# Kernel tuning notes

Measured on AMD Instinct MI355X. Metric: run time of the kernel, lower is better.

## Reference

```python
import jax, jax.numpy as jnp
import numpy as np

H = 16  # num_heads

def setup_inputs() -> dict:
    key = jax.random.key(0)
    k1, k2, k3 = jax.random.split(key, 3)
    D = 1024
    x = jax.random.normal(k1, (4, 2048, D), dtype=jnp.float32)
    W_qkv = jax.random.normal(k2, (D, 3 * D), dtype=jnp.float32) * (1.0 / np.sqrt(D))
    b_qkv = jnp.zeros((3 * D,), dtype=jnp.float32)
    W_out = jax.random.normal(k3, (D, D), dtype=jnp.float32) * (1.0 / np.sqrt(D))
    b_out = jnp.zeros((D,), dtype=jnp.float32)
    return {"x": x, "W_qkv": W_qkv, "b_qkv": b_qkv, "W_out": W_out, "b_out": b_out}

def reference(x, W_qkv, b_qkv, W_out, b_out):
    B, S, D = x.shape
    hd = D // H  # head_dim
    qkv = x @ W_qkv + b_qkv  # [B,S,3D]
    q, k, v = jnp.split(qkv, 3, axis=-1)
    # [B,S,D] -> [B,H,S,hd]
    q = q.reshape(B, S, H, hd).transpose(0, 2, 1, 3)
    k = k.reshape(B, S, H, hd).transpose(0, 2, 1, 3)
    v = v.reshape(B, S, H, hd).transpose(0, 2, 1, 3)
    scores = jnp.einsum('bhqd,bhkd->bhqk', q, k) / jnp.sqrt(jnp.float32(hd))
    weights = jax.nn.softmax(scores, axis=-1)  # dropout p=0.0 (eval)
    out = jnp.einsum('bhqk,bhkd->bhqd', weights, v)
    out = out.transpose(0, 2, 1, 3).reshape(B, S, D)
    return out @ W_out + b_out
```

## Files before the change

### kernel.cpp

```cpp
#include <hip/hip_runtime.h>

typedef __bf16 bf16;
typedef __bf16 bf16x8 __attribute__((ext_vector_type(8)));
typedef __bf16 bf16x4 __attribute__((ext_vector_type(4)));
typedef float f32x4 __attribute__((ext_vector_type(4)));

static constexpr int NB = 4;
static constexpr int NS = 2048;
static constexpr int ND = 1024;
static constexpr int NH = 16;
static constexpr int HD = 64;
static constexpr float QSCALE = 0.18033688011112042f;

#define GL16(g, l)                                                             \
    __builtin_amdgcn_global_load_lds(                                          \
        (const __attribute__((address_space(1))) void*)(g),                    \
        (__attribute__((address_space(3))) void*)(l), 16, 0, 0)

__global__ void k_conv(const float* __restrict__ in, bf16* __restrict__ out, int n) {
    int i = (blockIdx.x * blockDim.x + threadIdx.x) * 4;
    if (i < n) {
        float4 v = *reinterpret_cast<const float4*>(in + i);
        bf16* o = out + i;
        o[0] = (bf16)v.x; o[1] = (bf16)v.y; o[2] = (bf16)v.z; o[3] = (bf16)v.w;
    }
}

__global__ void k_transconv(const float* __restrict__ in, bf16* __restrict__ out,
                            int K, int N) {
    __shared__ float tile[32][33];
    int k0 = blockIdx.y * 32, n0 = blockIdx.x * 32;
    int tx = threadIdx.x, ty = threadIdx.y;
    for (int j = 0; j < 32; j += 8)
        tile[ty + j][tx] = in[(long)(k0 + ty + j) * N + n0 + tx];
    __syncthreads();
    for (int j = 0; j < 32; j += 8)
        out[(long)(n0 + ty + j) * K + k0 + tx] = (bf16)tile[tx][ty + j];
}

template <int EPI>
__global__ __launch_bounds__(256, 2) void k_gemm(
    const bf16* __restrict__ A, const bf16* __restrict__ Bt,
    const float* __restrict__ bias,
    void* __restrict__ out0, void* __restrict__ out1, void* __restrict__ out2,
    int M, int N, int Kd)
{
    constexpr int BM = 128, BN = 128, BK = 64;
    __shared__ __align__(16) bf16 As[2][BM * BK];
    __shared__ __align__(16) bf16 Bs[2][BN * BK];

    const int t = threadIdx.x;
    const int wid = t >> 6, lane = t & 63;
    const int wm = wid >> 1, wn = wid & 1;
    const int m0 = blockIdx.y * BM, n0 = blockIdx.x * BN;
    const int lrow = lane & 15, lhi = lane >> 4;

    const int srow0 = wid * 32 + (lane >> 3);
    const int scol = ((lane & 7) ^ (lane >> 3)) * 8;
    const bf16* ag = A + (long)(m0 + srow0) * Kd + scol;
    const bf16* bg = Bt + (long)(n0 + srow0) * Kd + scol;

    auto STAGE = [&](int buf_, int k0_) {
#pragma unroll
        for (int c = 0; c < 4; ++c) {
            GL16(ag + (long)(c * 8) * Kd + k0_, &As[buf_][(wid * 32 + c * 8) * BK]);
            GL16(bg + (long)(c * 8) * Kd + k0_, &Bs[buf_][(wid * 32 + c * 8) * BK]);
        }
    };

    f32x4 acc[4][4] = {};
    const int nt = Kd >> 6;
    const int swzr = (lrow & 7) << 4;
    int co[2];
#pragma unroll
    for (int kk = 0; kk < 2; ++kk)
        co[kk] = ((kk * 64 + lhi * 16) ^ swzr) >> 1;

    STAGE(0, 0);
    __syncthreads();
    int cur = 0;
    for (int tix = 0; tix < nt; ++tix) {
        if (tix + 1 < nt) STAGE(cur ^ 1, (tix + 1) * BK);

        bf16x8 af[2][4], bfr[2][4];
#pragma unroll
        for (int kk = 0; kk < 2; ++kk)
#pragma unroll
            for (int i = 0; i < 4; ++i) {
                af[kk][i]  = *reinterpret_cast<const bf16x8*>(
                    &As[cur][(wm * 64 + i * 16 + lrow) * BK + co[kk]]);
                bfr[kk][i] = *reinterpret_cast<const bf16x8*>(
                    &Bs[cur][(wn * 64 + i * 16 + lrow) * BK + co[kk]]);
            }
        __builtin_amdgcn_s_setprio(1);
#pragma unroll
        for (int kk = 0; kk < 2; ++kk)
#pragma unroll
            for (int i = 0; i < 4; ++i)
#pragma unroll
                for (int j = 0; j < 4; ++j)
                    acc[i][j] = __builtin_amdgcn_mfma_f32_16x16x32_bf16(
                        af[kk][i], bfr[kk][j], acc[i][j], 0, 0, 0);
        __builtin_amdgcn_s_setprio(0);
        __syncthreads();
        cur ^= 1;
    }

    if (EPI == 0) {
        bf16* Qb = (bf16*)out0; bf16* Kb = (bf16*)out1; bf16* Vt = (bf16*)out2;
#pragma unroll
        for (int j = 0; j < 4; ++j) {
            int col = n0 + wn * 64 + j * 16 + lrow;
            float bv = bias[col];
            int which = col >> 10;
            int rem = col & 1023;
            int h = rem >> 6, d = rem & 63;
#pragma unroll
            for (int i = 0; i < 4; ++i) {
                int mbase = m0 + wm * 64 + i * 16 + lhi * 4;
#pragma unroll
                for (int r = 0; r < 4; ++r) {
                    int row = mbase + r;
                    int bb = row >> 11, s = row & 2047;
                    long bh = bb * NH + h;
                    float v = acc[i][j][r] + bv;
                    if (which == 0)      Qb[(bh * NS + s) * HD + d] = (bf16)(v * QSCALE);
                    else if (which == 1) Kb[(bh * NS + s) * HD + d] = (bf16)v;
                    else                 Vt[(bh * HD + d) * NS + s] = (bf16)v;
                }
            }
        }
    } else {
        float* O = (float*)out0;
#pragma unroll
        for (int j = 0; j < 4; ++j) {
            int col = n0 + wn * 64 + j * 16 + lrow;
            float bv = bias[col];
#pragma unroll
            for (int i = 0; i < 4; ++i) {
                int mbase = m0 + wm * 64 + i * 16 + lhi * 4;
#pragma unroll
                for (int r = 0; r < 4; ++r)
                    O[(long)(mbase + r) * N + col] = acc[i][j][r] + bv;
            }
        }
    }
}

__global__ __launch_bounds__(256, 2) void k_attn(
    const bf16* __restrict__ Qb, const bf16* __restrict__ Kb,
    const bf16* __restrict__ Vt, bf16* __restrict__ Ao)
{
    constexpr int KB = 64;
    constexpr int NT = NS / KB;
    __shared__ bf16 Ks[2][KB * HD];
    __shared__ bf16 Vs[2][HD * KB];
    __shared__ bf16 Ps[4][16][72];

    const int t = threadIdx.x;
    const int wid = t >> 6, lane = t & 63;
    const int lrow = lane & 15, lhi = lane >> 4;

    const int flat = blockIdx.y * gridDim.x + blockIdx.x;
    const int n = (flat & 7) * 256 + (flat >> 3);
    const int bh = n >> 5;
    const int q0 = (n & 31) * 64 + wid * 16;

    const bf16* Qg = Qb + ((long)bh * NS + q0) * HD;
    const bf16* Kg = Kb + (long)bh * NS * HD;
    const bf16* Vg = Vt + (long)bh * HD * NS;

    bf16x8 qf[2];
#pragma unroll
    for (int c = 0; c < 2; ++c)
        qf[c] = *reinterpret_cast<const bf16x8*>(Qg + (long)lrow * HD + c * 32 + lhi * 8);

    f32x4 of[4] = {};
    float lsum = 0.f;

    const int sr  = t >> 2;
    const int scb = (t & 3) << 5;
    const int swz = (sr & 7) << 4;
    const int se0 = sr * 64 + ((scb ^ swz) >> 1);
    const int se1 = sr * 64 + (((scb + 16) ^ swz) >> 1);

    bf16x8 k0, k1, v0, v1;
#define LOADREGS(kb_)                                                          \
    {                                                                          \
        const bf16* kp = Kg + (long)((kb_) + sr) * HD + (scb >> 1);            \
        k0 = *reinterpret_cast<const bf16x8*>(kp);                             \
        k1 = *reinterpret_cast<const bf16x8*>(kp + 8);                         \
        const bf16* vp = Vg + (long)sr * NS + (kb_) + (scb >> 1);              \
        v0 = *reinterpret_cast<const bf16x8*>(vp);                             \
        v1 = *reinterpret_cast<const bf16x8*>(vp + 8);                         \
    }
#define WRITEBUF(b_)                                                           \
    {                                                                          \
        *reinterpret_cast<bf16x8*>(&Ks[b_][se0]) = k0;                         \
        *reinterpret_cast<bf16x8*>(&Ks[b_][se1]) = k1;                         \
        *reinterpret_cast<bf16x8*>(&Vs[b_][se0]) = v0;                         \
        *reinterpret_cast<bf16x8*>(&Vs[b_][se1]) = v1;                         \
    }

    LOADREGS(0);
    __syncthreads();
    WRITEBUF(0);
    LOADREGS(KB);

    for (int i = 0; i < NT; ++i) {
        __syncthreads();
        if (i + 1 < NT) WRITEBUF((i + 1) & 1);
        if (i + 2 < NT) LOADREGS((i + 2) * KB);
        const int b = i & 1;

        f32x4 st[4] = {};
        __builtin_amdgcn_s_setprio(1);
#pragma unroll
        for (int j = 0; j < 4; ++j) {
            const int row = j * 16 + lrow;
            const int rb = row * 64, rs = (row & 7) << 4;
#pragma unroll
            for (int c = 0; c < 2; ++c) {
                const int colb = c * 64 + lhi * 16;
                bf16x8 kf = *reinterpret_cast<const bf16x8*>(&Ks[b][rb + ((colb ^ rs) >> 1)]);
                st[j] = __builtin_amdgcn_mfma_f32_16x16x32_bf16(kf, qf[c], st[j], 0, 0, 0);
            }
        }
        __builtin_amdgcn_s_setprio(0);

#pragma unroll
        for (int j = 0; j < 4; ++j) {
            bf16x4 pk;
#pragma unroll
            for (int r = 0; r < 4; ++r) {
                float p = __builtin_amdgcn_exp2f(st[j][r]);
                lsum += p;
                pk[r] = (bf16)p;
            }
            *reinterpret_cast<bf16x4*>(&Ps[wid][lrow][j * 16 + 4 * lhi]) = pk;
        }

        __builtin_amdgcn_s_setprio(1);
#pragma unroll
        for (int chunk = 0; chunk < 2; ++chunk) {
            bf16x8 pf = *reinterpret_cast<const bf16x8*>(&Ps[wid][lrow][chunk * 32 + lhi * 8]);
#pragma unroll
            for (int f = 0; f < 4; ++f) {
                const int row = f * 16 + lrow;
                const int rb = row * 64, rs = (row & 7) << 4;
                const int colb = chunk * 64 + lhi * 16;
                bf16x8 vf = *reinterpret_cast<const bf16x8*>(&Vs[b][rb + ((colb ^ rs) >> 1)]);
                of[f] = __builtin_amdgcn_mfma_f32_16x16x32_bf16(pf, vf, of[f], 0, 0, 0);
            }
        }
        __builtin_amdgcn_s_setprio(0);
    }
#undef LOADREGS
#undef WRITEBUF

    lsum += __shfl_xor(lsum, 16);
    lsum += __shfl_xor(lsum, 32);
    float inv[4];
#pragma unroll
    for (int r = 0; r < 4; ++r)
        inv[r] = 1.0f / __shfl(lsum, 4 * lhi + r);

    const int bb = bh >> 4, h = bh & 15;
#pragma unroll
    for (int f = 0; f < 4; ++f) {
        int d = f * 16 + lrow;
#pragma unroll
        for (int r = 0; r < 4; ++r) {
            int s = q0 + 4 * lhi + r;
            Ao[((long)bb * NS + s) * ND + h * HD + d] = (bf16)(of[f][r] * inv[r]);
        }
    }
}

extern "C" void kernel_launch(void* const* d_in, const int* in_sizes, int n_in,
                              void* d_out, int out_size, void* d_ws, size_t ws_size,
                              hipStream_t stream) {
    const float* x    = (const float*)d_in[0];
    const float* Wqkv = (const float*)d_in[1];
    const float* bqkv = (const float*)d_in[2];
    const float* Wout = (const float*)d_in[3];
    const float* bout = (const float*)d_in[4];
    float* out = (float*)d_out;

    char* ws = (char*)d_ws;
    bf16* Xb  = (bf16*)(ws);
    bf16* Wqt = (bf16*)(ws + 16777216);
    bf16* Wot = (bf16*)(ws + 23068672);
    bf16* Qb  = (bf16*)(ws + 25165824);
    bf16* Kb  = (bf16*)(ws + 41943040);
    bf16* Vt  = (bf16*)(ws + 58720256);
    bf16* Ab  = (bf16*)(ws + 75497472);

    k_conv<<<dim3(8192), dim3(256), 0, stream>>>(x, Xb, NB * NS * ND);
    k_transconv<<<dim3(96, 32), dim3(32, 8), 0, stream>>>(Wqkv, Wqt, ND, 3 * ND);
    k_transconv<<<dim3(32, 32), dim3(32, 8), 0, stream>>>(Wout, Wot, ND, ND);

    k_gemm<0><<<dim3(24, 64), dim3(256), 0, stream>>>(
        Xb, Wqt, bqkv, Qb, Kb, Vt, NB * NS, 3 * ND, ND);

    k_attn<<<dim3(NS / 64, NB * NH), dim3(256), 0, stream>>>(Qb, Kb, Vt, Ab);

    k_gemm<1><<<dim3(8, 64), dim3(256), 0, stream>>>(
        Ab, Wot, bout, out, nullptr, nullptr, NB * NS, ND, ND);
}
```

Before: 224.3 us.

## Reshape P fragment in registers via permlane swaps instead of LDS round-trip

The attention kernel no longer writes exp'd scores to a shared-memory P buffer and reads them back as MFMA A-operand fragments. It packs pairs into bf16x2 words and rearranges them across lanes with permlane32_swap and xor-16 shuffles. This removes the per-tile LDS store/load and shared footprint, and launch bounds are raised to 4 blocks per SM to take advantage of the lower LDS use. In exchange it adds cross-lane shuffle instructions and tighter register limits, which could cause spills.

```diff
diff --git a/kernel.cpp b/kernel.cpp
--- a/kernel.cpp
+++ b/kernel.cpp
@@ -4,6 +4,7 @@
 typedef __bf16 bf16x8 __attribute__((ext_vector_type(8)));
 typedef __bf16 bf16x4 __attribute__((ext_vector_type(4)));
 typedef float f32x4 __attribute__((ext_vector_type(4)));
+typedef unsigned u32x2 __attribute__((ext_vector_type(2)));
 
 static constexpr int NB = 4;
 static constexpr int NS = 2048;
@@ -16,6 +17,12 @@
     __builtin_amdgcn_global_load_lds(                                          \
         (const __attribute__((address_space(1))) void*)(g),                    \
         (__attribute__((address_space(3))) void*)(l), 16, 0, 0)
+
+static __device__ __forceinline__ unsigned pk2(float a, float b) {
+    union { __bf16 h[2]; unsigned u; } t;
+    t.h[0] = (__bf16)a; t.h[1] = (__bf16)b;
+    return t.u;
+}
 
 __global__ void k_conv(const float* __restrict__ in, bf16* __restrict__ out, int n) {
     int i = (blockIdx.x * blockDim.x + threadIdx.x) * 4;
@@ -147,7 +154,7 @@
     }
 }
 
-__global__ __launch_bounds__(256, 2) void k_attn(
+__global__ __launch_bounds__(256, 4) void k_attn(
     const bf16* __restrict__ Qb, const bf16* __restrict__ Kb,
     const bf16* __restrict__ Vt, bf16* __restrict__ Ao)
 {
@@ -155,7 +162,6 @@
     constexpr int NT = NS / KB;
     __shared__ bf16 Ks[2][KB * HD];
     __shared__ bf16 Vs[2][HD * KB];
-    __shared__ bf16 Ps[4][16][72];
 
     const int t = threadIdx.x;
     const int wid = t >> 6, lane = t & 63;
@@ -228,32 +234,43 @@
         }
         __builtin_amdgcn_s_setprio(0);
 
+        unsigned pa[4], pb[4];
 #pragma unroll
         for (int j = 0; j < 4; ++j) {
-            bf16x4 pk;
-#pragma unroll
-            for (int r = 0; r < 4; ++r) {
-                float p = __builtin_amdgcn_exp2f(st[j][r]);
-                lsum += p;
-                pk[r] = (bf16)p;
-            }
-            *reinterpret_cast<bf16x4*>(&Ps[wid][lrow][j * 16 + 4 * lhi]) = pk;
-        }
-
-        __builtin_amdgcn_s_setprio(1);
-#pragma unroll
-        for (int chunk = 0; chunk < 2; ++chunk) {
-            bf16x8 pf = *reinterpret_cast<const bf16x8*>(&Ps[wid][lrow][chunk * 32 + lhi * 8]);
+            float e0 = __builtin_amdgcn_exp2f(st[j][0]);
+            float e1 = __builtin_amdgcn_exp2f(st[j][1]);
+            float e2 = __builtin_amdgcn_exp2f(st[j][2]);
+            float e3 = __builtin_amdgcn_exp2f(st[j][3]);
+            lsum += (e0 + e1) + (e2 + e3);
+            pa[j] = pk2(e0, e1);
+            pb[j] = pk2(e2, e3);
+        }
+
+        const bool sel = (lhi & 1) != 0;
+#pragma unroll
+        for (int c = 0; c < 2; ++c) {
+            u32x2 sa = __builtin_amdgcn_permlane32_swap(pa[2 * c], pa[2 * c + 1], false, false);
+            u32x2 sb = __builtin_amdgcn_permlane32_swap(pb[2 * c], pb[2 * c + 1], false, false);
+            unsigned Za = sa[0], Wa = sa[1], Zb = sb[0], Wb = sb[1];
+            unsigned Zas = __shfl_xor((int)Za, 16), Was = __shfl_xor((int)Wa, 16);
+            unsigned Zbs = __shfl_xor((int)Zb, 16), Wbs = __shfl_xor((int)Wb, 16);
+            union { unsigned u[4]; bf16x8 v; } frag;
+            frag.u[0] = sel ? Was : Za;
+            frag.u[1] = sel ? Wbs : Zb;
+            frag.u[2] = sel ? Wa : Zas;
+            frag.u[3] = sel ? Wb : Zbs;
+
+            __builtin_amdgcn_s_setprio(1);
 #pragma unroll
             for (int f = 0; f < 4; ++f) {
                 const int row = f * 16 + lrow;
                 const int rb = row * 64, rs = (row & 7) << 4;
-                const int colb = chunk * 64 + lhi * 16;
+                const int colb = c * 64 + lhi * 16;
                 bf16x8 vf = *reinterpret_cast<const bf16x8*>(&Vs[b][rb + ((colb ^ rs) >> 1)]);
-                of[f] = __builtin_amdgcn_mfma_f32_16x16x32_bf16(pf, vf, of[f], 0, 0, 0);
-            }
-        }
-        __builtin_amdgcn_s_setprio(0);
+                of[f] = __builtin_amdgcn_mfma_f32_16x16x32_bf16(frag.v, vf, of[f], 0, 0, 0);
+            }
+            __builtin_amdgcn_s_setprio(0);
+        }
     }
 #undef LOADREGS
 #undef WRITEBUF
```

New measurement: 232.5 us. 3.6% more time.

## Restructure attention: 32 queries per wave, async LDS staging, register-resident P

Applied to the files above, without the earlier changes.

The attention kernel now gives each wave 32 query rows instead of 16, so every K/V fragment read from LDS feeds two MFMAs. K/V tiles are staged straight into LDS with global_load_lds rather than through registers. P stays in registers and feeds 16x16x16 MFMAs, which removes the per-wave LDS round trip for P. Output stores are vectorised and launch bounds are raised to 4 blocks per CU. The cost is higher register pressure from doubled accumulators under the tighter occupancy bound, and a grid remap that halves the block count.

```diff
diff --git a/kernel.cpp b/kernel.cpp
--- a/kernel.cpp
+++ b/kernel.cpp
@@ -3,6 +3,7 @@
 typedef __bf16 bf16;
 typedef __bf16 bf16x8 __attribute__((ext_vector_type(8)));
 typedef __bf16 bf16x4 __attribute__((ext_vector_type(4)));
+typedef short s16x4 __attribute__((ext_vector_type(4)));
 typedef float f32x4 __attribute__((ext_vector_type(4)));
 
 static constexpr int NB = 4;
@@ -16,6 +17,12 @@
     __builtin_amdgcn_global_load_lds(                                          \
         (const __attribute__((address_space(1))) void*)(g),                    \
         (__attribute__((address_space(3))) void*)(l), 16, 0, 0)
+
+static __device__ __forceinline__ unsigned pk2(float a, float b) {
+    union { __bf16 h[2]; unsigned u; } t;
+    t.h[0] = (__bf16)a; t.h[1] = (__bf16)b;
+    return t.u;
+}
 
 __global__ void k_conv(const float* __restrict__ in, bf16* __restrict__ out, int n) {
     int i = (blockIdx.x * blockDim.x + threadIdx.x) * 4;
@@ -147,132 +154,130 @@
     }
 }
 
-__global__ __launch_bounds__(256, 2) void k_attn(
+__global__ __launch_bounds__(256, 4) void k_attn(
     const bf16* __restrict__ Qb, const bf16* __restrict__ Kb,
     const bf16* __restrict__ Vt, bf16* __restrict__ Ao)
 {
     constexpr int KB = 64;
     constexpr int NT = NS / KB;
-    __shared__ bf16 Ks[2][KB * HD];
-    __shared__ bf16 Vs[2][HD * KB];
-    __shared__ bf16 Ps[4][16][72];
+    __shared__ __align__(16) bf16 Ks[2][KB * HD];
+    __shared__ __align__(16) bf16 Vs[2][HD * KB];
 
     const int t = threadIdx.x;
     const int wid = t >> 6, lane = t & 63;
     const int lrow = lane & 15, lhi = lane >> 4;
 
     const int flat = blockIdx.y * gridDim.x + blockIdx.x;
-    const int n = (flat & 7) * 256 + (flat >> 3);
-    const int bh = n >> 5;
-    const int q0 = (n & 31) * 64 + wid * 16;
-
-    const bf16* Qg = Qb + ((long)bh * NS + q0) * HD;
+    const int n = (flat & 7) * 128 + (flat >> 3);
+    const int bh = n >> 4;
+    const int qblk = (n & 15) * 128;
+    const int qw = qblk + wid * 32;
+
+    const bf16* Qg = Qb + ((long)bh * NS + qw) * HD;
     const bf16* Kg = Kb + (long)bh * NS * HD;
     const bf16* Vg = Vt + (long)bh * HD * NS;
 
-    bf16x8 qf[2];
-#pragma unroll
-    for (int c = 0; c < 2; ++c)
-        qf[c] = *reinterpret_cast<const bf16x8*>(Qg + (long)lrow * HD + c * 32 + lhi * 8);
-
-    f32x4 of[4] = {};
-    float lsum = 0.f;
-
-    const int sr  = t >> 2;
-    const int scb = (t & 3) << 5;
-    const int swz = (sr & 7) << 4;
-    const int se0 = sr * 64 + ((scb ^ swz) >> 1);
-    const int se1 = sr * 64 + (((scb + 16) ^ swz) >> 1);
-
-    bf16x8 k0, k1, v0, v1;
-#define LOADREGS(kb_)                                                          \
+    bf16x8 qf[2][2];
+#pragma unroll
+    for (int qfr = 0; qfr < 2; ++qfr)
+#pragma unroll
+        for (int c = 0; c < 2; ++c)
+            qf[qfr][c] = *reinterpret_cast<const bf16x8*>(
+                Qg + (long)(qfr * 16 + lrow) * HD + c * 32 + lhi * 8);
+
+    f32x4 of[2][4] = {};
+    float lsum[2] = {0.f, 0.f};
+
+    const int gsr = lane >> 3;
+    const int gsc = ((lane & 7) ^ gsr) * 8;
+    auto STAGE = [&](int buf, int kb) {
+#pragma unroll
+        for (int c = 0; c < 2; ++c) {
+            const int rb = wid * 16 + c * 8;
+            GL16(Kg + (long)(kb + rb + gsr) * HD + gsc, &Ks[buf][rb * 64]);
+            GL16(Vg + (long)(rb + gsr) * NS + kb + gsc, &Vs[buf][rb * 64]);
+        }
+    };
+
+    const int rsw = (lrow & 7) << 4;
+
+#define COMPUTE(b_, i_)                                                        \
     {                                                                          \
-        const bf16* kp = Kg + (long)((kb_) + sr) * HD + (scb >> 1);            \
-        k0 = *reinterpret_cast<const bf16x8*>(kp);                             \
-        k1 = *reinterpret_cast<const bf16x8*>(kp + 8);                         \
-        const bf16* vp = Vg + (long)sr * NS + (kb_) + (scb >> 1);              \
-        v0 = *reinterpret_cast<const bf16x8*>(vp);                             \
-        v1 = *reinterpret_cast<const bf16x8*>(vp + 8);                         \
-    }
-#define WRITEBUF(b_)                                                           \
-    {                                                                          \
-        *reinterpret_cast<bf16x8*>(&Ks[b_][se0]) = k0;                         \
-        *reinterpret_cast<bf16x8*>(&Ks[b_][se1]) = k1;                         \
-        *reinterpret_cast<bf16x8*>(&Vs[b_][se0]) = v0;                         \
-        *reinterpret_cast<bf16x8*>(&Vs[b_][se1]) = v1;                         \
-    }
-
-    LOADREGS(0);
-    __syncthreads();
-    WRITEBUF(0);
-    LOADREGS(KB);
-
-    for (int i = 0; i < NT; ++i) {
+        f32x4 st[2][4] = {};                                                   \
+        __builtin_amdgcn_s_setprio(1);                                         \
+        _Pragma("unroll")                                                      \
+        for (int j = 0; j < 4; ++j) {                                          \
+            _Pragma("unroll")                                                  \
+            for (int c = 0; c < 2; ++c) {                                      \
+                bf16x8 kf = *reinterpret_cast<const bf16x8*>(                  \
+                    &Ks[b_][(j * 16 + lrow) * 64 +                             \
+                            (((c * 64 + lhi * 16) ^ rsw) >> 1)]);              \
+                _Pragma("unroll")                                              \
+                for (int qfr = 0; qfr < 2; ++qfr)                              \
+                    st[qfr][j] = __builtin_amdgcn_mfma_f32_16x16x32_bf16(      \
+                        kf, qf[qfr][c], st[qfr][j], 0, 0, 0);                  \
+            }                                                                  \
+        }                                                                      \
+        __builtin_amdgcn_s_setprio(0);                                         \
+        union { unsigned u[2]; s16x4 s; } pf[2][4];                            \
+        _Pragma("unroll")                                                      \
+        for (int qfr = 0; qfr < 2; ++qfr)                                      \
+            _Pragma("unroll")                                                  \
+            for (int j = 0; j < 4; ++j) {                                      \
+                float e0 = __builtin_amdgcn_exp2f(st[qfr][j][0]);              \
+                float e1 = __builtin_amdgcn_exp2f(st[qfr][j][1]);              \
+                float e2 = __builtin_amdgcn_exp2f(st[qfr][j][2]);              \
+                float e3 = __builtin_amdgcn_exp2f(st[qfr][j][3]);              \
+                lsum[qfr] += (e0 + e1) + (e2 + e3);                            \
+                pf[qfr][j].u[0] = pk2(e0, e1);                                 \
+                pf[qfr][j].u[1] = pk2(e2, e3);                                 \
+            }                                                                  \
+        __builtin_amdgcn_s_setprio(1);                                         \
+        _Pragma("unroll")                                                      \
+        for (int j = 0; j < 4; ++j) {                                          \
+            _Pragma("unroll")                                                  \
+            for (int f = 0; f < 4; ++f) {                                      \
+                s16x4 vf = *reinterpret_cast<const s16x4*>(                    \
+                    &Vs[b_][(f * 16 + lrow) * 64 +                             \
+                            (((j * 32 + lhi * 8) ^ rsw) >> 1)]);               \
+                _Pragma("unroll")                                              \
+                for (int qfr = 0; qfr < 2; ++qfr)                              \
+                    of[qfr][f] = __builtin_amdgcn_mfma_f32_16x16x16bf16_1k(    \
+                        vf, pf[qfr][j].s, of[qfr][f], 0, 0, 0);                \
+            }                                                                  \
+        }                                                                      \
+        __builtin_amdgcn_s_setprio(0);                                         \
+    }
+
+    STAGE(0, 0);
+    for (int it = 0; it < NT; it += 2) {
         __syncthreads();
-        if (i + 1 < NT) WRITEBUF((i + 1) & 1);
-        if (i + 2 < NT) LOADREGS((i + 2) * KB);
-        const int b = i & 1;
-
-        f32x4 st[4] = {};
-        __builtin_amdgcn_s_setprio(1);
-#pragma unroll
-        for (int j = 0; j < 4; ++j) {
-            const int row = j * 16 + lrow;
-            const int rb = row * 64, rs = (row & 7) << 4;
-#pragma unroll
-            for (int c = 0; c < 2; ++c) {
-                const int colb = c * 64 + lhi * 16;
-                bf16x8 kf = *reinterpret_cast<const bf16x8*>(&Ks[b][rb + ((colb ^ rs) >> 1)]);
-                st[j] = __builtin_amdgcn_mfma_f32_16x16x32_bf16(kf, qf[c], st[j], 0, 0, 0);
-            }
-        }
-        __builtin_amdgcn_s_setprio(0);
-
-#pragma unroll
-        for (int j = 0; j < 4; ++j) {
-            bf16x4 pk;
-#pragma unroll
-            for (int r = 0; r < 4; ++r) {
-                float p = __builtin_amdgcn_exp2f(st[j][r]);
-                lsum += p;
-                pk[r] = (bf16)p;
-            }
-            *reinterpret_cast<bf16x4*>(&Ps[wid][lrow][j * 16 + 4 * lhi]) = pk;
-        }
-
-        __builtin_amdgcn_s_setprio(1);
-#pragma unroll
-        for (int chunk = 0; chunk < 2; ++chunk) {
-            bf16x8 pf = *reinterpret_cast<const bf16x8*>(&Ps[wid][lrow][chunk * 32 + lhi * 8]);
-#pragma unroll
-            for (int f = 0; f < 4; ++f) {
-                const int row = f * 16 + lrow;
-                const int rb = row * 64, rs = (row & 7) << 4;
-                const int colb = chunk * 64 + lhi * 16;
-                bf16x8 vf = *reinterpret_cast<const bf16x8*>(&Vs[b][rb + ((colb ^ rs) >> 1)]);
-                of[f] = __builtin_amdgcn_mfma_f32_16x16x32_bf16(pf, vf, of[f], 0, 0, 0);
-            }
-        }
-        __builtin_amdgcn_s_setprio(0);
-    }
-#undef LOADREGS
-#undef WRITEBUF
-
-    lsum += __shfl_xor(lsum, 16);
-    lsum += __shfl_xor(lsum, 32);
-    float inv[4];
-#pragma unroll
-    for (int r = 0; r < 4; ++r)
-        inv[r] = 1.0f / __shfl(lsum, 4 * lhi + r);
+        STAGE(1, (it + 1) * KB);
+        COMPUTE(0, it);
+        __syncthreads();
+        if (it + 2 < NT) STAGE(0, (it + 2) * KB);
+        COMPUTE(1, it + 1);
+    }
+#undef COMPUTE
+
+#pragma unroll
+    for (int qfr = 0; qfr < 2; ++qfr) {
+        lsum[qfr] += __shfl_xor(lsum[qfr], 16);
+        lsum[qfr] += __shfl_xor(lsum[qfr], 32);
+    }
 
     const int bb = bh >> 4, h = bh & 15;
 #pragma unroll
-    for (int f = 0; f < 4; ++f) {
-        int d = f * 16 + lrow;
-#pragma unroll
-        for (int r = 0; r < 4; ++r) {
-            int s = q0 + 4 * lhi + r;
-            Ao[((long)bb * NS + s) * ND + h * HD + d] = (bf16)(of[f][r] * inv[r]);
+    for (int qfr = 0; qfr < 2; ++qfr) {
+        float inv = 1.0f / lsum[qfr];
+        int s = qw + qfr * 16 + lrow;
+#pragma unroll
+        for (int f = 0; f < 4; ++f) {
+            bf16x4 o4;
+#pragma unroll
+            for (int r = 0; r < 4; ++r) o4[r] = (bf16)(of[qfr][f][r] * inv);
+            *reinterpret_cast<bf16x4*>(
+                &Ao[((long)bb * NS + s) * ND + h * HD + f * 16 + 4 * lhi]) = o4;
         }
     }
 }
@@ -303,7 +308,7 @@
     k_gemm<0><<<dim3(24, 64), dim3(256), 0, stream>>>(
         Xb, Wqt, bqkv, Qb, Kb, Vt, NB * NS, 3 * ND, ND);
 
-    k_attn<<<dim3(NS / 64, NB * NH), dim3(256), 0, stream>>>(Qb, Kb, Vt, Ab);
+    k_attn<<<dim3(16, 64), dim3(256), 0, stream>>>(Qb, Kb, Vt, Ab);
 
     k_gemm<1><<<dim3(8, 64), dim3(256), 0, stream>>>(
         Ab, Wot, bout, out, nullptr, nullptr, NB * NS, ND, ND);
```

New measurement: 233.2 us. +4.0%, slower.
